# Kernel tuning notes

Hardware: AMD Instinct MI355X
Metric: run time of the kernel (lower is better)

Reference implementation:

```python
import jax, jax.numpy as jnp
import numpy as np

EPS = 1e-8


def setup_inputs() -> dict:
    key = jax.random.key(0)
    k1, k2, k3, k4 = jax.random.split(key, 4)
    N, E, d = 10000, 5000, 128
    F = jax.random.normal(k1, (N, d), dtype=jnp.float32)
    H = jax.random.uniform(k2, (N, E), dtype=jnp.float32)
    Dv = jax.random.uniform(k3, (N, N), dtype=jnp.float32)
    De = jax.random.uniform(k4, (E, E), dtype=jnp.float32)
    return {"F": F, "H": H, "Dv": Dv, "De": De}


def reference(F, H, Dv, De):
    # Only the diagonals of Dv/De are used by the original (torch.diag extraction).
    dv = jnp.diagonal(Dv)                      # [N]
    de = jnp.diagonal(De)                      # [E]
    dv_inv_sqrt = (dv + EPS) ** -0.5           # diag of Dv^{-1/2}
    de_inv = 1.0 / (de + EPS)                  # diag of De^{-1}
    # L = I - Dv^{-1/2} H De^{-1} H^T Dv^{-1/2}
    # trace(F^T L F) = ||F||_F^2 - sum_e de_inv[e] * ||(H^T (Dv^{-1/2} F))[e]||^2
    Fs = F * dv_inv_sqrt[:, None]              # [N, d]
    M = H.T @ Fs                               # [E, d]
    trace_term = jnp.sum(F * F) - jnp.sum(de_inv[:, None] * (M * M))
    # use_rayleigh=False; reduction='mean' -> divide by N
    loss = trace_term / F.shape[0]
    return loss
```

## Files before the change

kernel.cpp:

```cpp
#include <hip/hip_runtime.h>

#define EPSF 1e-8f

typedef __attribute__((ext_vector_type(8))) short bf16x8;
typedef __attribute__((ext_vector_type(4))) float f32x4;

constexpr int Nv     = 10000;
constexpr int Ne     = 5000;
constexpr int Dd     = 128;
constexpr int NPAD   = 10016;
constexpr int EPAD   = 5120;
constexpr int KSTEPS = 313;
constexpr int KSPLIT = 12;

__device__ __forceinline__ unsigned short f2bf_rne(float f) {
    unsigned int u = __builtin_bit_cast(unsigned int, f);
    u += 0x7fffu + ((u >> 16) & 1u);
    return (unsigned short)(u >> 16);
}

__global__ void prep_dv_kernel(const float* __restrict__ Dv, float* __restrict__ dvis) {
    int n = blockIdx.x * 256 + threadIdx.x;
    if (n < NPAD) dvis[n] = (n < Nv) ? rsqrtf(Dv[(size_t)n * (Nv + 1)] + EPSF) : 0.0f;
}

__global__ void prep_fst_kernel(const float* __restrict__ F, const float* __restrict__ dvis,
                                short* __restrict__ Fst) {
    int n = blockIdx.x * 256 + threadIdx.x;
    int c = blockIdx.y;
    if (n < NPAD) {
        unsigned short b = 0;
        if (n < Nv) b = f2bf_rne(F[(size_t)n * Dd + c] * dvis[n]);
        Fst[(size_t)c * NPAD + n] = (short)b;
    }
}

__global__ void sum_ff_kernel(const float* __restrict__ F, float* __restrict__ out0) {
    const float4* F4 = (const float4*)F;
    int base = blockIdx.x * 512 + threadIdx.x;
    float4 a = F4[base];
    float4 b = F4[base + 256];
    float sum = a.x*a.x + a.y*a.y + a.z*a.z + a.w*a.w
              + b.x*b.x + b.y*b.y + b.z*b.z + b.w*b.w;
    #pragma unroll
    for (int off = 32; off; off >>= 1) sum += __shfl_down(sum, off);
    if ((threadIdx.x & 63) == 0) atomicAdd(out0, sum);
}

__global__ __launch_bounds__(512, 4)
void gemm_split_kernel(const float* __restrict__ H, const short* __restrict__ Fst,
                       float* __restrict__ Mp) {
    __shared__ unsigned int Alds[2][128 * 20];

    const int t   = threadIdx.x;
    const int w   = t >> 6;
    const int l   = t & 63;
    const int lm  = l & 15;
    const int q   = l >> 4;
    const int e0  = blockIdx.x * 128;
    const int we  = (w >> 1) * 32;
    const int wc  = (w & 1) * 64;
    const int spl = blockIdx.y;
    const int sb  = (spl * KSTEPS) / KSPLIT;
    const int se  = ((spl + 1) * KSTEPS) / KSPLIT;

    const int rp  = t & 15;
    const int cpb = t >> 4;

    float2 hcur[2][2], hnxt[2][2];

    auto loadH = [&](int s, float2 (&h)[2][2]) {
        const int n = s * 32 + 2 * rp;
        #pragma unroll
        for (int j = 0; j < 2; ++j) {
            const int el = 2 * (cpb + 32 * j);
            const int e  = e0 + el;
            h[j][0] = make_float2(0.f, 0.f);
            h[j][1] = make_float2(0.f, 0.f);
            if (n < Nv && e < Ne) {
                h[j][0] = *(const float2*)(H + (size_t)n * Ne + e);
                h[j][1] = *(const float2*)(H + (size_t)(n + 1) * Ne + e);
            }
        }
    };
    auto writeLDS = [&](int buf, float2 (&h)[2][2]) {
        #pragma unroll
        for (int j = 0; j < 2; ++j) {
            const int el = 2 * (cpb + 32 * j);
            unsigned int w0 = (unsigned int)f2bf_rne(h[j][0].x) | ((unsigned int)f2bf_rne(h[j][1].x) << 16);
            unsigned int w1 = (unsigned int)f2bf_rne(h[j][0].y) | ((unsigned int)f2bf_rne(h[j][1].y) << 16);
            Alds[buf][el * 20 + rp]       = w0;
            Alds[buf][(el + 1) * 20 + rp] = w1;
        }
    };

    f32x4 acc[2][4];
    #pragma unroll
    for (int a = 0; a < 2; ++a)
        #pragma unroll
        for (int b = 0; b < 4; ++b) acc[a][b] = (f32x4){0.f, 0.f, 0.f, 0.f};

    loadH(sb, hcur);
    writeLDS(0, hcur);
    __syncthreads();

    for (int s = sb; s < se; ++s) {
        const int buf = (s - sb) & 1;
        const int n0  = s * 32;

        if (s + 1 < se) loadH(s + 1, hnxt);

        bf16x8 Bf[4];
        #pragma unroll
        for (int cb = 0; cb < 4; ++cb) {
            const int c = wc + cb * 16 + lm;
            Bf[cb] = *(const bf16x8*)(Fst + (size_t)c * NPAD + n0 + q * 8);
        }
        bf16x8 Af[2];
        #pragma unroll
        for (int eb = 0; eb < 2; ++eb) {
            const int el = we + eb * 16 + lm;
            Af[eb] = *(const bf16x8*)((const char*)Alds[buf] + el * 80 + q * 16);
        }

        #pragma unroll
        for (int cb = 0; cb < 4; ++cb)
            #pragma unroll
            for (int eb = 0; eb < 2; ++eb)
                acc[eb][cb] = __builtin_amdgcn_mfma_f32_16x16x32_bf16(
                    Af[eb], Bf[cb], acc[eb][cb], 0, 0, 0);

        if (s + 1 < se) writeLDS(buf ^ 1, hnxt);
        __syncthreads();
    }

    float* dst = Mp + (size_t)spl * EPAD * 128;
    #pragma unroll
    for (int eb = 0; eb < 2; ++eb) {
        #pragma unroll
        for (int cb = 0; cb < 4; ++cb) {
            const int c = wc + cb * 16 + lm;
            #pragma unroll
            for (int r = 0; r < 4; ++r) {
                const int el = we + eb * 16 + q * 4 + r;
                dst[(size_t)(e0 + el) * 128 + c] = acc[eb][cb][r];
            }
        }
    }
}

__global__ void reduce_m_kernel(const float* __restrict__ Mp, const float* __restrict__ De,
                                float* __restrict__ outS) {
    int gid = blockIdx.x * 256 + threadIdx.x;
    int e   = gid >> 5;
    int c4  = (gid & 31) * 4;
    float de_inv = (e < Ne) ? 1.0f / (De[(size_t)e * (Ne + 1)] + EPSF) : 0.0f;
    float4 m = {0.f, 0.f, 0.f, 0.f};
    #pragma unroll
    for (int sp = 0; sp < KSPLIT; ++sp) {
        float4 p = *(const float4*)(Mp + (size_t)sp * EPAD * 128 + (size_t)e * 128 + c4);
        m.x += p.x; m.y += p.y; m.z += p.z; m.w += p.w;
    }
    float sum = de_inv * (m.x*m.x + m.y*m.y + m.z*m.z + m.w*m.w);
    #pragma unroll
    for (int off = 32; off; off >>= 1) sum += __shfl_down(sum, off);
    if ((threadIdx.x & 63) == 0) atomicAdd(outS, sum);
}

__global__ void final_kernel(const float* __restrict__ ws0, float* __restrict__ out) {
    out[0] = (ws0[0] - ws0[1]) * (1.0f / (float)Nv);
}

extern "C" void kernel_launch(void* const* d_in, const int* in_sizes, int n_in,
                              void* d_out, int out_size, void* d_ws, size_t ws_size,
                              hipStream_t stream) {
    (void)in_sizes; (void)n_in; (void)out_size; (void)ws_size;
    const float* F  = (const float*)d_in[0];
    const float* H  = (const float*)d_in[1];
    const float* Dv = (const float*)d_in[2];
    const float* De = (const float*)d_in[3];
    float* out = (float*)d_out;

    float* ws0  = (float*)d_ws;
    float* dvis = ws0 + 16;
    float* Mp   = dvis + NPAD;
    short* Fst  = (short*)(Mp + (size_t)KSPLIT * EPAD * 128);

    hipMemsetAsync(ws0, 0, 64, stream);

    prep_dv_kernel <<<(NPAD + 255) / 256, 256, 0, stream>>>(Dv, dvis);
    prep_fst_kernel<<<dim3((NPAD + 255) / 256, 128), 256, 0, stream>>>(F, dvis, Fst);
    sum_ff_kernel  <<<625, 256, 0, stream>>>(F, ws0);
    gemm_split_kernel<<<dim3(EPAD / 128, KSPLIT), 512, 0, stream>>>(H, Fst, Mp);
    reduce_m_kernel<<<640, 256, 0, stream>>>(Mp, De, ws0 + 1);
    final_kernel   <<<1, 1, 0, stream>>>(ws0, out);
}
```

Baseline: 703.2 us.

## Double K-tile to 64 rows and prefetch H two stages ahead

```diff
diff --git a/kernel.cpp b/kernel.cpp
--- a/kernel.cpp
+++ b/kernel.cpp
@@ -8,9 +8,9 @@
 constexpr int Nv     = 10000;
 constexpr int Ne     = 5000;
 constexpr int Dd     = 128;
-constexpr int NPAD   = 10016;
+constexpr int NPAD   = 10048;
 constexpr int EPAD   = 5120;
-constexpr int KSTEPS = 313;
+constexpr int KSTEPS = 157;
 constexpr int KSPLIT = 12;
 
 __device__ __forceinline__ unsigned short f2bf_rne(float f) {
@@ -50,7 +50,7 @@
 __global__ __launch_bounds__(512, 4)
 void gemm_split_kernel(const float* __restrict__ H, const short* __restrict__ Fst,
                        float* __restrict__ Mp) {
-    __shared__ unsigned int Alds[2][128 * 20];
+    __shared__ unsigned int Alds[2][128 * 36];
 
     const int t   = threadIdx.x;
     const int w   = t >> 6;
@@ -67,30 +67,36 @@
     const int rp  = t & 15;
     const int cpb = t >> 4;
 
-    float2 hcur[2][2], hnxt[2][2];
-
-    auto loadH = [&](int s, float2 (&h)[2][2]) {
-        const int n = s * 32 + 2 * rp;
-        #pragma unroll
-        for (int j = 0; j < 2; ++j) {
-            const int el = 2 * (cpb + 32 * j);
-            const int e  = e0 + el;
-            h[j][0] = make_float2(0.f, 0.f);
-            h[j][1] = make_float2(0.f, 0.f);
-            if (n < Nv && e < Ne) {
-                h[j][0] = *(const float2*)(H + (size_t)n * Ne + e);
-                h[j][1] = *(const float2*)(H + (size_t)(n + 1) * Ne + e);
+    float2 hA[2][2][2], hB[2][2][2];
+
+    auto loadH = [&](int s, float2 (&h)[2][2][2]) {
+        #pragma unroll
+        for (int jj = 0; jj < 2; ++jj) {
+            const int n = s * 64 + 32 * jj + 2 * rp;
+            #pragma unroll
+            for (int j = 0; j < 2; ++j) {
+                const int e = e0 + 2 * (cpb + 32 * j);
+                h[jj][j][0] = make_float2(0.f, 0.f);
+                h[jj][j][1] = make_float2(0.f, 0.f);
+                if (n < Nv && e < Ne) {
+                    h[jj][j][0] = *(const float2*)(H + (size_t)n * Ne + e);
+                    h[jj][j][1] = *(const float2*)(H + (size_t)(n + 1) * Ne + e);
+                }
             }
         }
     };
-    auto writeLDS = [&](int buf, float2 (&h)[2][2]) {
-        #pragma unroll
-        for (int j = 0; j < 2; ++j) {
-            const int el = 2 * (cpb + 32 * j);
-            unsigned int w0 = (unsigned int)f2bf_rne(h[j][0].x) | ((unsigned int)f2bf_rne(h[j][1].x) << 16);
-            unsigned int w1 = (unsigned int)f2bf_rne(h[j][0].y) | ((unsigned int)f2bf_rne(h[j][1].y) << 16);
-            Alds[buf][el * 20 + rp]       = w0;
-            Alds[buf][(el + 1) * 20 + rp] = w1;
+    auto writeLDS = [&](int buf, float2 (&h)[2][2][2]) {
+        #pragma unroll
+        for (int jj = 0; jj < 2; ++jj) {
+            const int kp = rp + 16 * jj;
+            #pragma unroll
+            for (int j = 0; j < 2; ++j) {
+                const int el = 2 * (cpb + 32 * j);
+                unsigned int w0 = (unsigned int)f2bf_rne(h[jj][j][0].x) | ((unsigned int)f2bf_rne(h[jj][j][1].x) << 16);
+                unsigned int w1 = (unsigned int)f2bf_rne(h[jj][j][0].y) | ((unsigned int)f2bf_rne(h[jj][j][1].y) << 16);
+                Alds[buf][el * 36 + kp]       = w0;
+                Alds[buf][(el + 1) * 36 + kp] = w1;
+            }
         }
     };
 
@@ -100,38 +106,51 @@
         #pragma unroll
         for (int b = 0; b < 4; ++b) acc[a][b] = (f32x4){0.f, 0.f, 0.f, 0.f};
 
-    loadH(sb, hcur);
-    writeLDS(0, hcur);
+    auto compute = [&](int buf, int s) {
+        #pragma unroll
+        for (int h = 0; h < 2; ++h) {
+            const int n0 = s * 64 + 32 * h + q * 8;
+            bf16x8 Bf[4];
+            #pragma unroll
+            for (int cb = 0; cb < 4; ++cb) {
+                const int c = wc + cb * 16 + lm;
+                Bf[cb] = *(const bf16x8*)(Fst + (size_t)c * NPAD + n0);
+            }
+            bf16x8 Af[2];
+            #pragma unroll
+            for (int eb = 0; eb < 2; ++eb) {
+                const int el = we + eb * 16 + lm;
+                Af[eb] = *(const bf16x8*)((const char*)Alds[buf] + el * 144 + h * 64 + q * 16);
+            }
+            #pragma unroll
+            for (int cb = 0; cb < 4; ++cb)
+                #pragma unroll
+                for (int eb = 0; eb < 2; ++eb)
+                    acc[eb][cb] = __builtin_amdgcn_mfma_f32_16x16x32_bf16(
+                        Af[eb], Bf[cb], acc[eb][cb], 0, 0, 0);
+        }
+    };
+
+    loadH(sb, hA);
+    writeLDS(0, hA);
+    loadH(sb + 1, hB);
     __syncthreads();
 
-    for (int s = sb; s < se; ++s) {
-        const int buf = (s - sb) & 1;
-        const int n0  = s * 32;
-
-        if (s + 1 < se) loadH(s + 1, hnxt);
-
-        bf16x8 Bf[4];
-        #pragma unroll
-        for (int cb = 0; cb < 4; ++cb) {
-            const int c = wc + cb * 16 + lm;
-            Bf[cb] = *(const bf16x8*)(Fst + (size_t)c * NPAD + n0 + q * 8);
-        }
-        bf16x8 Af[2];
-        #pragma unroll
-        for (int eb = 0; eb < 2; ++eb) {
-            const int el = we + eb * 16 + lm;
-            Af[eb] = *(const bf16x8*)((const char*)Alds[buf] + el * 80 + q * 16);
-        }
-
-        #pragma unroll
-        for (int cb = 0; cb < 4; ++cb)
-            #pragma unroll
-            for (int eb = 0; eb < 2; ++eb)
-                acc[eb][cb] = __builtin_amdgcn_mfma_f32_16x16x32_bf16(
-                    Af[eb], Bf[cb], acc[eb][cb], 0, 0, 0);
-
-        if (s + 1 < se) writeLDS(buf ^ 1, hnxt);
+    int s = sb, buf = 0;
+    while (true) {
+        if (s + 2 < se) loadH(s + 2, hA);
+        compute(buf, s);
+        if (s + 1 < se) writeLDS(buf ^ 1, hB);
         __syncthreads();
+        ++s; buf ^= 1;
+        if (s >= se) break;
+
+        if (s + 2 < se) loadH(s + 2, hB);
+        compute(buf, s);
+        if (s + 1 < se) writeLDS(buf ^ 1, hA);
+        __syncthreads();
+        ++s; buf ^= 1;
+        if (s >= se) break;
     }
 
     float* dst = Mp + (size_t)spl * EPAD * 128;
```

Result: slower. 718.3 us (+2.2%).

## Vectorize H loads to float4, XOR-swizzle LDS tile, fuse sum(F^2) into prep

Applied to the files above, without the earlier changes.

```diff
diff --git a/kernel.cpp b/kernel.cpp
--- a/kernel.cpp
+++ b/kernel.cpp
@@ -25,26 +25,22 @@
 }
 
 __global__ void prep_fst_kernel(const float* __restrict__ F, const float* __restrict__ dvis,
-                                short* __restrict__ Fst) {
+                                short* __restrict__ Fst, float* __restrict__ out0) {
     int n = blockIdx.x * 256 + threadIdx.x;
     int c = blockIdx.y;
+    float v = 0.0f;
     if (n < NPAD) {
         unsigned short b = 0;
-        if (n < Nv) b = f2bf_rne(F[(size_t)n * Dd + c] * dvis[n]);
+        if (n < Nv) {
+            float f = F[(size_t)n * Dd + c];
+            v = f * f;
+            b = f2bf_rne(f * dvis[n]);
+        }
         Fst[(size_t)c * NPAD + n] = (short)b;
     }
-}
-
-__global__ void sum_ff_kernel(const float* __restrict__ F, float* __restrict__ out0) {
-    const float4* F4 = (const float4*)F;
-    int base = blockIdx.x * 512 + threadIdx.x;
-    float4 a = F4[base];
-    float4 b = F4[base + 256];
-    float sum = a.x*a.x + a.y*a.y + a.z*a.z + a.w*a.w
-              + b.x*b.x + b.y*b.y + b.z*b.z + b.w*b.w;
     #pragma unroll
-    for (int off = 32; off; off >>= 1) sum += __shfl_down(sum, off);
-    if ((threadIdx.x & 63) == 0) atomicAdd(out0, sum);
+    for (int off = 32; off; off >>= 1) v += __shfl_down(v, off);
+    if ((threadIdx.x & 63) == 0) atomicAdd(out0, v);
 }
 
 __global__ __launch_bounds__(512, 4)
@@ -64,33 +60,30 @@
     const int sb  = (spl * KSTEPS) / KSPLIT;
     const int se  = ((spl + 1) * KSTEPS) / KSPLIT;
 
-    const int rp  = t & 15;
-    const int cpb = t >> 4;
+    const int p   = t >> 5;
+    const int bcl = t & 31;
+    const int ecol = e0 + 4 * bcl;
 
-    float2 hcur[2][2], hnxt[2][2];
+    float4 hcur[2], hnxt[2];
 
-    auto loadH = [&](int s, float2 (&h)[2][2]) {
-        const int n = s * 32 + 2 * rp;
-        #pragma unroll
-        for (int j = 0; j < 2; ++j) {
-            const int el = 2 * (cpb + 32 * j);
-            const int e  = e0 + el;
-            h[j][0] = make_float2(0.f, 0.f);
-            h[j][1] = make_float2(0.f, 0.f);
-            if (n < Nv && e < Ne) {
-                h[j][0] = *(const float2*)(H + (size_t)n * Ne + e);
-                h[j][1] = *(const float2*)(H + (size_t)(n + 1) * Ne + e);
-            }
+    auto loadH = [&](int s, float4 (&h)[2]) {
+        const int n = s * 32 + 2 * p;
+        h[0] = make_float4(0.f, 0.f, 0.f, 0.f);
+        h[1] = make_float4(0.f, 0.f, 0.f, 0.f);
+        if (n < Nv && ecol < Ne) {
+            h[0] = *(const float4*)(H + (size_t)n * Ne + ecol);
+            h[1] = *(const float4*)(H + (size_t)(n + 1) * Ne + ecol);
         }
     };
-    auto writeLDS = [&](int buf, float2 (&h)[2][2]) {
+    auto writeLDS = [&](int buf, float4 (&h)[2]) {
+        const float a0[4] = {h[0].x, h[0].y, h[0].z, h[0].w};
+        const float a1[4] = {h[1].x, h[1].y, h[1].z, h[1].w};
         #pragma unroll
-        for (int j = 0; j < 2; ++j) {
-            const int el = 2 * (cpb + 32 * j);
-            unsigned int w0 = (unsigned int)f2bf_rne(h[j][0].x) | ((unsigned int)f2bf_rne(h[j][1].x) << 16);
-            unsigned int w1 = (unsigned int)f2bf_rne(h[j][0].y) | ((unsigned int)f2bf_rne(h[j][1].y) << 16);
-            Alds[buf][el * 20 + rp]       = w0;
-            Alds[buf][(el + 1) * 20 + rp] = w1;
+        for (int j = 0; j < 4; ++j) {
+            const int el = 4 * bcl + j;
+            unsigned int wv = (unsigned int)f2bf_rne(a0[j]) | ((unsigned int)f2bf_rne(a1[j]) << 16);
+            const int idx = (el * 20 + p) ^ (((el >> 3) & 7) << 2);
+            Alds[buf][idx] = wv;
         }
     };
 
@@ -120,7 +113,8 @@
         #pragma unroll
         for (int eb = 0; eb < 2; ++eb) {
             const int el = we + eb * 16 + lm;
-            Af[eb] = *(const bf16x8*)((const char*)Alds[buf] + el * 80 + q * 16);
+            const int boff = (el * 80 + q * 16) ^ (((el >> 3) & 7) << 4);
+            Af[eb] = *(const bf16x8*)((const char*)Alds[buf] + boff);
         }
 
         #pragma unroll
@@ -189,8 +183,7 @@
     hipMemsetAsync(ws0, 0, 64, stream);
 
     prep_dv_kernel <<<(NPAD + 255) / 256, 256, 0, stream>>>(Dv, dvis);
-    prep_fst_kernel<<<dim3((NPAD + 255) / 256, 128), 256, 0, stream>>>(F, dvis, Fst);
-    sum_ff_kernel  <<<625, 256, 0, stream>>>(F, ws0);
+    prep_fst_kernel<<<dim3((NPAD + 255) / 256, 128), 256, 0, stream>>>(F, dvis, Fst, ws0);
     gemm_split_kernel<<<dim3(EPAD / 128, KSPLIT), 512, 0, stream>>>(H, Fst, Mp);
     reduce_m_kernel<<<640, 256, 0, stream>>>(Mp, De, ws0 + 1);
     final_kernel   <<<1, 1, 0, stream>>>(ws0, out);
```

New measurement: 922.9 us. 31.3% more time.
